# Optimization experiments

Hardware: AMD Instinct MI355X
Metric: run time of the kernel (lower is better)

Reference implementation:

```python
import jax, jax.numpy as jnp
import numpy as np

B, P, C = 1024, 64, 512  # batch, patnum, d_model(channels)
LN_EPS = 1e-5

def setup_inputs() -> dict:
    key = jax.random.key(0)
    k = jax.random.split(key, 5)
    s = 1.0 / np.sqrt(P)  # torch Linear default init scale
    x  = jax.random.normal(k[0], (B, P, C), dtype=jnp.float32)
    W1 = jax.random.uniform(k[1], (C, P, P), minval=-s, maxval=s, dtype=jnp.float32)
    b1 = jax.random.uniform(k[2], (C, P),   minval=-s, maxval=s, dtype=jnp.float32)
    W2 = jax.random.uniform(k[3], (C, P, P), minval=-s, maxval=s, dtype=jnp.float32)
    b2 = jax.random.uniform(k[4], (C, P),   minval=-s, maxval=s, dtype=jnp.float32)
    gamma = jnp.ones((C,), dtype=jnp.float32)   # LayerNorm weight
    beta  = jnp.zeros((C,), dtype=jnp.float32)  # LayerNorm bias
    return {"x": x, "W1": W1, "b1": b1, "W2": W2, "b2": b2, "gamma": gamma, "beta": beta}

def reference(x, W1, b1, W2, b2, gamma, beta):
    # Per-channel Linear over the patch dim, batched across channels.
    # torch Linear: y[q] = sum_p x[p] * W[q, p] + b[q]
    h = jnp.einsum('bpc,cqp->bqc', x, W1) + b1.T[None]          # [B, P, C]
    h = jax.nn.gelu(h, approximate=False)                        # exact GELU (torch default)
    o = jnp.einsum('bpc,cqp->bqc', h, W2) + b2.T[None]          # [B, P, C]
    # Dropout is identity in eval; residual + LayerNorm over channel dim.
    res = o + x
    mean = jnp.mean(res, axis=-1, keepdims=True)
    var = jnp.mean((res - mean) ** 2, axis=-1, keepdims=True)
    return (res - mean) * jax.lax.rsqrt(var + LN_EPS) * gamma + beta
```

## Files before the change

kernel.cpp:

```cpp
#include <hip/hip_runtime.h>
#include <cstdint>
#include <cstddef>

#define BB 1024
#define PP 64
#define CC 512
#define MM (BB * PP)
constexpr float LN_EPS = 1e-5f;

typedef short  s16x8 __attribute__((ext_vector_type(8)));
typedef float  f32x4 __attribute__((ext_vector_type(4)));
typedef unsigned int u32x2 __attribute__((ext_vector_type(2)));

__device__ __forceinline__ unsigned cvt_pk_bf16(float lo, float hi) {
    unsigned r;
    asm("v_cvt_pk_bf16_f32 %0, %1, %2" : "=v"(r) : "v"(lo), "v"(hi));
    return r;
}
__device__ __forceinline__ unsigned cvt_pk_f16(float lo, float hi) {
    unsigned r;
    asm("v_cvt_pkrtz_f16_f32 %0, %1, %2" : "=v"(r) : "v"(lo), "v"(hi));
    return r;
}
__device__ __forceinline__ float h2f(unsigned short h) {
    float f;
    asm("v_cvt_f32_f16 %0, %1" : "=v"(f) : "v"((unsigned)h));
    return f;
}
__device__ __forceinline__ float bflo(unsigned u) { union { unsigned u; float f; } v; v.u = u << 16;          return v.f; }
__device__ __forceinline__ float bfhi(unsigned u) { union { unsigned u; float f; } v; v.u = u & 0xffff0000u;  return v.f; }

__device__ __forceinline__ s16x8 ldwf(const float* p) {
    float4 a = *(const float4*)p;
    float4 b = *(const float4*)(p + 4);
    union { s16x8 v; unsigned u[4]; } r;
    r.u[0] = cvt_pk_bf16(a.x, a.y);
    r.u[1] = cvt_pk_bf16(a.z, a.w);
    r.u[2] = cvt_pk_bf16(b.x, b.y);
    r.u[3] = cvt_pk_bf16(b.z, b.w);
    return r.v;
}

__device__ __forceinline__ float gelu_t(float t) {
    float sg = 1.5957691216f * (t + 0.044715f * t * t * t);
    return t / (1.0f + __expf(-sg));
}

__device__ __forceinline__ void lds_barrier() {
    asm volatile("s_waitcnt lgkmcnt(0)" ::: "memory");
    __builtin_amdgcn_s_barrier();
}

template<int HALF>
__global__ __launch_bounds__(1024, 4) void k_mix_rt(
    const float* __restrict__ X,  const float* __restrict__ W1,
    const float* __restrict__ B1, const float* __restrict__ W2,
    const float* __restrict__ B2, void* __restrict__ RTv)
{
    __shared__ __align__(16) unsigned short XS[16 * 1160];
    __shared__ __align__(16) unsigned short HS[16 * 1152];
    __shared__ __align__(16) float          BS[16 * 128];

    const int tid  = threadIdx.x;
    const int lane = tid & 63;
    const int wv   = tid >> 6;
    const int lb   = lane & 15;
    const int lq   = lane >> 4;

    const int gid = blockIdx.x;
    const int cg  = gid & 31;
    const int bt  = gid >> 5;
    const int c0  = cg * 16, b0 = bt * 128;
    const int c   = c0 + wv;

    const float* w1c = W1 + (size_t)c * 4096;
    const float* w2c = W2 + (size_t)c * 4096;
    const int wq = lb * 64 + lq * 8;
    s16x8 w1_0_0 = ldwf(w1c +    0 + wq), w1_0_1 = ldwf(w1c +    0 + wq + 32);
    s16x8 w1_1_0 = ldwf(w1c + 1024 + wq), w1_1_1 = ldwf(w1c + 1024 + wq + 32);
    s16x8 w1_2_0 = ldwf(w1c + 2048 + wq), w1_2_1 = ldwf(w1c + 2048 + wq + 32);
    s16x8 w1_3_0 = ldwf(w1c + 3072 + wq), w1_3_1 = ldwf(w1c + 3072 + wq + 32);
    s16x8 w2_0_0 = ldwf(w2c +    0 + wq), w2_0_1 = ldwf(w2c +    0 + wq + 32);
    s16x8 w2_1_0 = ldwf(w2c + 1024 + wq), w2_1_1 = ldwf(w2c + 1024 + wq + 32);
    s16x8 w2_2_0 = ldwf(w2c + 2048 + wq), w2_2_1 = ldwf(w2c + 2048 + wq + 32);
    s16x8 w2_3_0 = ldwf(w2c + 3072 + wq), w2_3_1 = ldwf(w2c + 3072 + wq + 32);

    BS[wv * 128 +      lane] = B1[c * 64 + lane];
    BS[wv * 128 + 64 + lane] = B2[c * 64 + lane];

    const unsigned short* xp = &XS[wv * 1160];
    unsigned short*       hp = &HS[wv * 1152];

    const int sc4 = tid & 3;
    const int sp2 = (tid >> 2) & 31;
    const int sbo = tid >> 7;

    float4 r0[2], r1[2];
    #pragma unroll
    for (int pass = 0; pass < 2; ++pass) {
        const float* src = X + ((size_t)(b0 + pass * 8 + sbo) * PP + 2 * sp2) * CC
                             + c0 + sc4 * 4;
        r0[pass] = *(const float4*)src;
        r1[pass] = *(const float4*)(src + CC);
    }

    for (int s = 0; s < 8; ++s) {
        const int bb = b0 + s * 16;

        #pragma unroll
        for (int pass = 0; pass < 2; ++pass) {
            int b = pass * 8 + sbo;
            *(unsigned*)&XS[(sc4 * 4 + 0) * 1160 + b * 72 + 2 * sp2] = cvt_pk_bf16(r0[pass].x, r1[pass].x);
            *(unsigned*)&XS[(sc4 * 4 + 1) * 1160 + b * 72 + 2 * sp2] = cvt_pk_bf16(r0[pass].y, r1[pass].y);
            *(unsigned*)&XS[(sc4 * 4 + 2) * 1160 + b * 72 + 2 * sp2] = cvt_pk_bf16(r0[pass].z, r1[pass].z);
            *(unsigned*)&XS[(sc4 * 4 + 3) * 1160 + b * 72 + 2 * sp2] = cvt_pk_bf16(r0[pass].w, r1[pass].w);
        }

        if (s < 7) {
            #pragma unroll
            for (int pass = 0; pass < 2; ++pass) {
                const float* src = X + ((size_t)(bb + 16 + pass * 8 + sbo) * PP + 2 * sp2) * CC
                                     + c0 + sc4 * 4;
                r0[pass] = *(const float4*)src;
                r1[pass] = *(const float4*)(src + CC);
            }
        }
        lds_barrier();

        s16x8 xf0 = *(const s16x8*)(xp + lb * 72 +  0 + lq * 8);
        s16x8 xf1 = *(const s16x8*)(xp + lb * 72 + 32 + lq * 8);

        #define DO1(mt) { \
            float4 bv = *(const float4*)&BS[wv * 128 + mt * 16 + lq * 4]; \
            f32x4 a = {bv.x, bv.y, bv.z, bv.w}; \
            a = __builtin_amdgcn_mfma_f32_16x16x32_bf16(w1_##mt##_0, xf0, a, 0, 0, 0); \
            a = __builtin_amdgcn_mfma_f32_16x16x32_bf16(w1_##mt##_1, xf1, a, 0, 0, 0); \
            u32x2 hpk; \
            hpk[0] = cvt_pk_bf16(gelu_t(a[0]), gelu_t(a[1])); \
            hpk[1] = cvt_pk_bf16(gelu_t(a[2]), gelu_t(a[3])); \
            *(u32x2*)(hp + lb * 72 + mt * 16 + lq * 4) = hpk; }
        DO1(0) DO1(1) DO1(2) DO1(3)
        #undef DO1

        u32x2 xv0 = *(const u32x2*)(xp + lb * 72 +  0 + lq * 4);
        u32x2 xv1 = *(const u32x2*)(xp + lb * 72 + 16 + lq * 4);
        u32x2 xv2 = *(const u32x2*)(xp + lb * 72 + 32 + lq * 4);
        u32x2 xv3 = *(const u32x2*)(xp + lb * 72 + 48 + lq * 4);

        asm volatile("s_waitcnt lgkmcnt(0)" ::: "memory");

        s16x8 hf0 = *(const s16x8*)(hp + lb * 72 +  0 + lq * 8);
        s16x8 hf1 = *(const s16x8*)(hp + lb * 72 + 32 + lq * 8);

        const size_t rbase = (size_t)c * MM + (size_t)(bb + lb) * 64 + lq * 4;
        #define DO2(mt) { \
            float4 bv = *(const float4*)&BS[wv * 128 + 64 + mt * 16 + lq * 4]; \
            f32x4 a = {bv.x, bv.y, bv.z, bv.w}; \
            a = __builtin_amdgcn_mfma_f32_16x16x32_bf16(w2_##mt##_0, hf0, a, 0, 0, 0); \
            a = __builtin_amdgcn_mfma_f32_16x16x32_bf16(w2_##mt##_1, hf1, a, 0, 0, 0); \
            a[0] += bflo(xv##mt[0]); a[1] += bfhi(xv##mt[0]); \
            a[2] += bflo(xv##mt[1]); a[3] += bfhi(xv##mt[1]); \
            if constexpr (!HALF) { \
                *(f32x4*)((float*)RTv + rbase + mt * 16) = a; \
            } else { \
                u32x2 hv; \
                hv[0] = cvt_pk_f16(a[0], a[1]); \
                hv[1] = cvt_pk_f16(a[2], a[3]); \
                *(u32x2*)((unsigned short*)RTv + rbase + mt * 16) = hv; \
            } }
        DO2(0) DO2(1) DO2(2) DO2(3)
        #undef DO2

        lds_barrier();
    }
}

template<int HALF>
__global__ __launch_bounds__(1024, 4) void k_ln_rt(
    const void* __restrict__ RTv, float* __restrict__ OUT,
    const float* __restrict__ G,  const float* __restrict__ Be)
{
    __shared__ float S[64][516];
    __shared__ float pS[16][64];
    __shared__ float pQ[16][64];
    __shared__ float mu_s[64], inv_s[64];
    __shared__ float gS[512], bS[512];

    const int tid = threadIdx.x;
    const int colbase = blockIdx.x * 64;

    if (tid < 512) gS[tid] = G[tid];
    else           bS[tid - 512] = Be[tid - 512];

    #pragma unroll
    for (int pass = 0; pass < 8; ++pass) {
        const int cc = pass * 64 + (tid >> 4);
        const int ch = (tid & 15) * 4;
        float v0, v1, v2, v3;
        if constexpr (!HALF) {
            f32x4 v = *(const f32x4*)((const float*)RTv + (size_t)cc * MM + colbase + ch);
            v0 = v[0]; v1 = v[1]; v2 = v[2]; v3 = v[3];
        } else {
            u32x2 v = *(const u32x2*)((const unsigned short*)RTv + (size_t)cc * MM + colbase + ch);
            v0 = h2f((unsigned short)(v[0] & 0xffff)); v1 = h2f((unsigned short)(v[0] >> 16));
            v2 = h2f((unsigned short)(v[1] & 0xffff)); v3 = h2f((unsigned short)(v[1] >> 16));
        }
        S[ch + 0][cc] = v0; S[ch + 1][cc] = v1;
        S[ch + 2][cc] = v2; S[ch + 3][cc] = v3;
    }
    __syncthreads();

    const int col = tid >> 4;
    const int cs  = tid & 15;
    float sum = 0.f, sq = 0.f;
    #pragma unroll
    for (int j = 0; j < 32; ++j) {
        float v = S[col][j * 16 + cs];
        sum += v; sq += v * v;
    }
    pS[cs][col] = sum; pQ[cs][col] = sq;
    __syncthreads();

    if (tid < 64) {
        float s = 0.f, q = 0.f;
        #pragma unroll
        for (int k = 0; k < 16; ++k) { s += pS[k][tid]; q += pQ[k][tid]; }
        const float mu  = s * (1.0f / CC);
        const float var = q * (1.0f / CC) - mu * mu;
        mu_s[tid]  = mu;
        inv_s[tid] = rsqrtf(var + LN_EPS);
    }
    __syncthreads();

    const int pos = tid & 7;
    const int hs  = (tid >> 3) & 1;
    const float mu  = mu_s[col];
    const float inv = inv_s[col];
    float* orow = OUT + (size_t)(colbase + col) * CC;
    #pragma unroll
    for (int k = 0; k < 8; ++k) {
        const int cc = hs * 256 + k * 32 + pos * 4;
        f32x4 v = *(const f32x4*)&S[col][cc];
        f32x4 o;
        o[0] = (v[0] - mu) * inv * gS[cc + 0] + bS[cc + 0];
        o[1] = (v[1] - mu) * inv * gS[cc + 1] + bS[cc + 1];
        o[2] = (v[2] - mu) * inv * gS[cc + 2] + bS[cc + 2];
        o[3] = (v[3] - mu) * inv * gS[cc + 3] + bS[cc + 3];
        *(f32x4*)(orow + cc) = o;
    }
}

__global__ __launch_bounds__(1024) void k_mix_legacy(
    const float* __restrict__ X,  const float* __restrict__ W1,
    const float* __restrict__ B1, const float* __restrict__ W2,
    const float* __restrict__ B2, float* __restrict__ OUT)
{
    __shared__ __align__(16) unsigned short XS[16 * 1160];
    __shared__ __align__(16) unsigned short HS[16 * 1152];
    __shared__ __align__(16) float          RS[16 * 1092];
    __shared__ __align__(16) float          BS[16 * 128];

    const int tid  = threadIdx.x;
    const int lane = tid & 63;
    const int wv   = tid >> 6;
    const int lb   = lane & 15;
    const int lq   = lane >> 4;

    const int gid = blockIdx.x;
    const int cg  = gid & 31;
    const int bt  = gid >> 5;
    const int c0  = cg * 16, b0 = bt * 128;
    const int c   = c0 + wv;

    const float* w1c = W1 + (size_t)c * 4096;
    const float* w2c = W2 + (size_t)c * 4096;
    const int wq = lb * 64 + lq * 8;
    s16x8 w1_0_0 = ldwf(w1c +    0 + wq), w1_0_1 = ldwf(w1c +    0 + wq + 32);
    s16x8 w1_1_0 = ldwf(w1c + 1024 + wq), w1_1_1 = ldwf(w1c + 1024 + wq + 32);
    s16x8 w1_2_0 = ldwf(w1c + 2048 + wq), w1_2_1 = ldwf(w1c + 2048 + wq + 32);
    s16x8 w1_3_0 = ldwf(w1c + 3072 + wq), w1_3_1 = ldwf(w1c + 3072 + wq + 32);
    s16x8 w2_0_0 = ldwf(w2c +    0 + wq), w2_0_1 = ldwf(w2c +    0 + wq + 32);
    s16x8 w2_1_0 = ldwf(w2c + 1024 + wq), w2_1_1 = ldwf(w2c + 1024 + wq + 32);
    s16x8 w2_2_0 = ldwf(w2c + 2048 + wq), w2_2_1 = ldwf(w2c + 2048 + wq + 32);
    s16x8 w2_3_0 = ldwf(w2c + 3072 + wq), w2_3_1 = ldwf(w2c + 3072 + wq + 32);

    BS[wv * 128 +      lane] = B1[c * 64 + lane];
    BS[wv * 128 + 64 + lane] = B2[c * 64 + lane];

    const unsigned short* xp = &XS[wv * 1160];
    unsigned short*       hp = &HS[wv * 1152];

    const int sc4 = tid & 3;
    const int sp2 = (tid >> 2) & 31;
    const int sbo = tid >> 7;

    float4 r0[2], r1[2];
    #pragma unroll
    for (int pass = 0; pass < 2; ++pass) {
        const float* src = X + ((size_t)(b0 + pass * 8 + sbo) * PP + 2 * sp2) * CC
                             + c0 + sc4 * 4;
        r0[pass] = *(const float4*)src;
        r1[pass] = *(const float4*)(src + CC);
    }

    for (int s = 0; s < 8; ++s) {
        const int bb = b0 + s * 16;
        #pragma unroll
        for (int pass = 0; pass < 2; ++pass) {
            int b = pass * 8 + sbo;
            *(unsigned*)&XS[(sc4 * 4 + 0) * 1160 + b * 72 + 2 * sp2] = cvt_pk_bf16(r0[pass].x, r1[pass].x);
            *(unsigned*)&XS[(sc4 * 4 + 1) * 1160 + b * 72 + 2 * sp2] = cvt_pk_bf16(r0[pass].y, r1[pass].y);
            *(unsigned*)&XS[(sc4 * 4 + 2) * 1160 + b * 72 + 2 * sp2] = cvt_pk_bf16(r0[pass].z, r1[pass].z);
            *(unsigned*)&XS[(sc4 * 4 + 3) * 1160 + b * 72 + 2 * sp2] = cvt_pk_bf16(r0[pass].w, r1[pass].w);
        }
        __syncthreads();
        if (s < 7) {
            #pragma unroll
            for (int pass = 0; pass < 2; ++pass) {
                const float* src = X + ((size_t)(bb + 16 + pass * 8 + sbo) * PP + 2 * sp2) * CC
                                     + c0 + sc4 * 4;
                r0[pass] = *(const float4*)src;
                r1[pass] = *(const float4*)(src + CC);
            }
        }
        s16x8 xf0 = *(const s16x8*)(xp + lb * 72 +  0 + lq * 8);
        s16x8 xf1 = *(const s16x8*)(xp + lb * 72 + 32 + lq * 8);
        #define DO1(mt) { \
            float4 bv = *(const float4*)&BS[wv * 128 + mt * 16 + lq * 4]; \
            f32x4 a = {bv.x, bv.y, bv.z, bv.w}; \
            a = __builtin_amdgcn_mfma_f32_16x16x32_bf16(w1_##mt##_0, xf0, a, 0, 0, 0); \
            a = __builtin_amdgcn_mfma_f32_16x16x32_bf16(w1_##mt##_1, xf1, a, 0, 0, 0); \
            u32x2 hpk; \
            hpk[0] = cvt_pk_bf16(gelu_t(a[0]), gelu_t(a[1])); \
            hpk[1] = cvt_pk_bf16(gelu_t(a[2]), gelu_t(a[3])); \
            *(u32x2*)(hp + lb * 72 + mt * 16 + lq * 4) = hpk; }
        DO1(0) DO1(1) DO1(2) DO1(3)
        #undef DO1
        asm volatile("s_waitcnt lgkmcnt(0)" ::: "memory");
        s16x8 hf0 = *(const s16x8*)(hp + lb * 72 +  0 + lq * 8);
        s16x8 hf1 = *(const s16x8*)(hp + lb * 72 + 32 + lq * 8);
        #define DO2(mt) { \
            float4 bv = *(const float4*)&BS[wv * 128 + 64 + mt * 16 + lq * 4]; \
            f32x4 a = {bv.x, bv.y, bv.z, bv.w}; \
            a = __builtin_amdgcn_mfma_f32_16x16x32_bf16(w2_##mt##_0, hf0, a, 0, 0, 0); \
            a = __builtin_amdgcn_mfma_f32_16x16x32_bf16(w2_##mt##_1, hf1, a, 0, 0, 0); \
            u32x2 xv = *(const u32x2*)(xp + lb * 72 + mt * 16 + lq * 4); \
            a[0] += bflo(xv[0]); a[1] += bfhi(xv[0]); \
            a[2] += bflo(xv[1]); a[3] += bfhi(xv[1]); \
            *(f32x4*)&RS[lb * 1092 + wv * 68 + mt * 16 + lq * 4] = a; }
        DO2(0) DO2(1) DO2(2) DO2(3)
        #undef DO2
        __syncthreads();
        #pragma unroll
        for (int it = 0; it < 4; ++it) {
            int fi = it * 1024 + tid;
            int c4 = fi & 3, q = (fi >> 2) & 63, b = fi >> 8;
            const float* rp = &RS[b * 1092 + c4 * 4 * 68 + q];
            float4 v = { rp[0], rp[68], rp[136], rp[204] };
            *(float4*)(OUT + ((size_t)(bb + b) * PP + q) * CC + c0 + c4 * 4) = v;
        }
    }
}

__global__ __launch_bounds__(256) void k_ln_legacy(
    float* __restrict__ OUT, const float* __restrict__ G, const float* __restrict__ Be)
{
    const int lane = threadIdx.x & 63;
    const int m    = blockIdx.x * 4 + (threadIdx.x >> 6);
    float4* row = (float4*)(OUT + (size_t)m * CC);
    float4 v0 = row[lane], v1 = row[lane + 64];
    float s = (v0.x + v0.y) + (v0.z + v0.w) + (v1.x + v1.y) + (v1.z + v1.w);
    float q = (v0.x * v0.x + v0.y * v0.y) + (v0.z * v0.z + v0.w * v0.w)
            + (v1.x * v1.x + v1.y * v1.y) + (v1.z * v1.z + v1.w * v1.w);
    #pragma unroll
    for (int o = 32; o >= 1; o >>= 1) {
        s += __shfl_xor(s, o, 64);
        q += __shfl_xor(q, o, 64);
    }
    const float mu  = s * (1.0f / CC);
    const float var = q * (1.0f / CC) - mu * mu;
    const float inv = rsqrtf(var + LN_EPS);
    const float4 g0 = ((const float4*)G)[lane],  g1 = ((const float4*)G)[lane + 64];
    const float4 e0 = ((const float4*)Be)[lane], e1 = ((const float4*)Be)[lane + 64];
    v0.x = (v0.x - mu) * inv * g0.x + e0.x;  v0.y = (v0.y - mu) * inv * g0.y + e0.y;
    v0.z = (v0.z - mu) * inv * g0.z + e0.z;  v0.w = (v0.w - mu) * inv * g0.w + e0.w;
    v1.x = (v1.x - mu) * inv * g1.x + e1.x;  v1.y = (v1.y - mu) * inv * g1.y + e1.y;
    v1.z = (v1.z - mu) * inv * g1.z + e1.z;  v1.w = (v1.w - mu) * inv * g1.w + e1.w;
    row[lane] = v0; row[lane + 64] = v1;
}

extern "C" void kernel_launch(void* const* d_in, const int* in_sizes, int n_in,
                              void* d_out, int out_size, void* d_ws, size_t ws_size,
                              hipStream_t stream) {
    const float* X  = (const float*)d_in[0];
    const float* W1 = (const float*)d_in[1];
    const float* B1 = (const float*)d_in[2];
    const float* W2 = (const float*)d_in[3];
    const float* B2 = (const float*)d_in[4];
    const float* G  = (const float*)d_in[5];
    const float* Be = (const float*)d_in[6];
    float* OUT = (float*)d_out;

    const size_t need32 = (size_t)CC * MM * sizeof(float);
    const size_t need16 = (size_t)CC * MM * sizeof(unsigned short);

    if (d_ws && ws_size >= need32) {
        k_mix_rt<0><<<256, 1024, 0, stream>>>(X, W1, B1, W2, B2, d_ws);
        k_ln_rt<0><<<MM / 64, 1024, 0, stream>>>(d_ws, OUT, G, Be);
    } else if (d_ws && ws_size >= need16) {
        k_mix_rt<1><<<256, 1024, 0, stream>>>(X, W1, B1, W2, B2, d_ws);
        k_ln_rt<1><<<MM / 64, 1024, 0, stream>>>(d_ws, OUT, G, Be);
    } else {
        k_mix_legacy<<<256, 1024, 0, stream>>>(X, W1, B1, W2, B2, OUT);
        k_ln_legacy<<<MM / 4, 256, 0, stream>>>(OUT, G, Be);
    }
}
```

Measured before the change: 339.9 us.

## Pre-transpose X to channel-major bf16 in a separate kernel before the mixer

Adds a transpose kernel that converts X to bf16 and writes it channel-major into the workspace. The mixer then reads each channel's activations straight from global memory instead of staging them through shared memory, which removes the LDS staging and the block barriers. The mixer block shrinks to 4 waves with biases kept in registers. The cost is an extra kernel launch plus an extra write and read of a 64 MB bf16 intermediate. The transpose's strided 2-byte global stores may also be poorly coalesced.

```diff
diff --git a/kernel.cpp b/kernel.cpp
--- a/kernel.cpp
+++ b/kernel.cpp
@@ -46,20 +46,40 @@
     return t / (1.0f + __expf(-sg));
 }
 
-__device__ __forceinline__ void lds_barrier() {
-    asm volatile("s_waitcnt lgkmcnt(0)" ::: "memory");
-    __builtin_amdgcn_s_barrier();
+__global__ __launch_bounds__(1024, 4) void k_tr(
+    const float* __restrict__ X, unsigned short* __restrict__ XT)
+{
+    __shared__ unsigned short S[64 * 514];
+    const int tid = threadIdx.x;
+    const int mb  = blockIdx.x;
+    const int rg  = tid >> 7;
+    const int c0  = (tid & 127) * 4;
+
+    #pragma unroll
+    for (int it = 0; it < 8; ++it) {
+        const int m = it * 8 + rg;
+        float4 v = *(const float4*)(X + (size_t)(mb * 64 + m) * CC + c0);
+        unsigned* p = (unsigned*)&S[m * 514 + c0];
+        p[0] = cvt_pk_bf16(v.x, v.y);
+        p[1] = cvt_pk_bf16(v.z, v.w);
+    }
+    __syncthreads();
+
+    const int wv = tid >> 6, lane = tid & 63;
+    unsigned short* dst = XT + (size_t)(wv * 32) * MM + mb * 64 + lane;
+    #pragma unroll
+    for (int j = 0; j < 32; ++j) {
+        dst[(size_t)j * MM] = S[lane * 514 + wv * 32 + j];
+    }
 }
 
 template<int HALF>
-__global__ __launch_bounds__(1024, 4) void k_mix_rt(
-    const float* __restrict__ X,  const float* __restrict__ W1,
+__global__ __launch_bounds__(256, 3) void k_mix_rt(
+    const unsigned short* __restrict__ XT, const float* __restrict__ W1,
     const float* __restrict__ B1, const float* __restrict__ W2,
     const float* __restrict__ B2, void* __restrict__ RTv)
 {
-    __shared__ __align__(16) unsigned short XS[16 * 1160];
-    __shared__ __align__(16) unsigned short HS[16 * 1152];
-    __shared__ __align__(16) float          BS[16 * 128];
+    __shared__ __align__(16) unsigned short HS[4][1152];
 
     const int tid  = threadIdx.x;
     const int lane = tid & 63;
@@ -68,10 +88,10 @@
     const int lq   = lane >> 4;
 
     const int gid = blockIdx.x;
-    const int cg  = gid & 31;
-    const int bt  = gid >> 5;
-    const int c0  = cg * 16, b0 = bt * 128;
-    const int c   = c0 + wv;
+    const int cgi = gid & 127;
+    const int bt  = gid >> 7;
+    const int c   = cgi * 4 + wv;
+    const int b0  = bt * 128;
 
     const float* w1c = W1 + (size_t)c * 4096;
     const float* w2c = W2 + (size_t)c * 4096;
@@ -84,55 +104,31 @@
     s16x8 w2_1_0 = ldwf(w2c + 1024 + wq), w2_1_1 = ldwf(w2c + 1024 + wq + 32);
     s16x8 w2_2_0 = ldwf(w2c + 2048 + wq), w2_2_1 = ldwf(w2c + 2048 + wq + 32);
     s16x8 w2_3_0 = ldwf(w2c + 3072 + wq), w2_3_1 = ldwf(w2c + 3072 + wq + 32);
-
-    BS[wv * 128 +      lane] = B1[c * 64 + lane];
-    BS[wv * 128 + 64 + lane] = B2[c * 64 + lane];
-
-    const unsigned short* xp = &XS[wv * 1160];
-    unsigned short*       hp = &HS[wv * 1152];
-
-    const int sc4 = tid & 3;
-    const int sp2 = (tid >> 2) & 31;
-    const int sbo = tid >> 7;
-
-    float4 r0[2], r1[2];
-    #pragma unroll
-    for (int pass = 0; pass < 2; ++pass) {
-        const float* src = X + ((size_t)(b0 + pass * 8 + sbo) * PP + 2 * sp2) * CC
-                             + c0 + sc4 * 4;
-        r0[pass] = *(const float4*)src;
-        r1[pass] = *(const float4*)(src + CC);
-    }
+    const float4 b1_0 = *(const float4*)(B1 + c * 64 +  0 + lq * 4);
+    const float4 b1_1 = *(const float4*)(B1 + c * 64 + 16 + lq * 4);
+    const float4 b1_2 = *(const float4*)(B1 + c * 64 + 32 + lq * 4);
+    const float4 b1_3 = *(const float4*)(B1 + c * 64 + 48 + lq * 4);
+    const float4 b2_0 = *(const float4*)(B2 + c * 64 +  0 + lq * 4);
+    const float4 b2_1 = *(const float4*)(B2 + c * 64 + 16 + lq * 4);
+    const float4 b2_2 = *(const float4*)(B2 + c * 64 + 32 + lq * 4);
+    const float4 b2_3 = *(const float4*)(B2 + c * 64 + 48 + lq * 4);
+
+    const unsigned short* xtc = XT + (size_t)c * MM;
+    unsigned short*       hp  = &HS[wv][0];
 
     for (int s = 0; s < 8; ++s) {
         const int bb = b0 + s * 16;
-
-        #pragma unroll
-        for (int pass = 0; pass < 2; ++pass) {
-            int b = pass * 8 + sbo;
-            *(unsigned*)&XS[(sc4 * 4 + 0) * 1160 + b * 72 + 2 * sp2] = cvt_pk_bf16(r0[pass].x, r1[pass].x);
-            *(unsigned*)&XS[(sc4 * 4 + 1) * 1160 + b * 72 + 2 * sp2] = cvt_pk_bf16(r0[pass].y, r1[pass].y);
-            *(unsigned*)&XS[(sc4 * 4 + 2) * 1160 + b * 72 + 2 * sp2] = cvt_pk_bf16(r0[pass].z, r1[pass].z);
-            *(unsigned*)&XS[(sc4 * 4 + 3) * 1160 + b * 72 + 2 * sp2] = cvt_pk_bf16(r0[pass].w, r1[pass].w);
-        }
-
-        if (s < 7) {
-            #pragma unroll
-            for (int pass = 0; pass < 2; ++pass) {
-                const float* src = X + ((size_t)(bb + 16 + pass * 8 + sbo) * PP + 2 * sp2) * CC
-                                     + c0 + sc4 * 4;
-                r0[pass] = *(const float4*)src;
-                r1[pass] = *(const float4*)(src + CC);
-            }
-        }
-        lds_barrier();
-
-        s16x8 xf0 = *(const s16x8*)(xp + lb * 72 +  0 + lq * 8);
-        s16x8 xf1 = *(const s16x8*)(xp + lb * 72 + 32 + lq * 8);
+        const unsigned short* xrow = xtc + (size_t)(bb + lb) * 64;
+
+        s16x8 xf0 = *(const s16x8*)(xrow +      lq * 8);
+        s16x8 xf1 = *(const s16x8*)(xrow + 32 + lq * 8);
+        u32x2 xv0 = *(const u32x2*)(xrow +  0 + lq * 4);
+        u32x2 xv1 = *(const u32x2*)(xrow + 16 + lq * 4);
+        u32x2 xv2 = *(const u32x2*)(xrow + 32 + lq * 4);
+        u32x2 xv3 = *(const u32x2*)(xrow + 48 + lq * 4);
 
         #define DO1(mt) { \
-            float4 bv = *(const float4*)&BS[wv * 128 + mt * 16 + lq * 4]; \
-            f32x4 a = {bv.x, bv.y, bv.z, bv.w}; \
+            f32x4 a = {b1_##mt.x, b1_##mt.y, b1_##mt.z, b1_##mt.w}; \
             a = __builtin_amdgcn_mfma_f32_16x16x32_bf16(w1_##mt##_0, xf0, a, 0, 0, 0); \
             a = __builtin_amdgcn_mfma_f32_16x16x32_bf16(w1_##mt##_1, xf1, a, 0, 0, 0); \
             u32x2 hpk; \
@@ -142,11 +138,6 @@
         DO1(0) DO1(1) DO1(2) DO1(3)
         #undef DO1
 
-        u32x2 xv0 = *(const u32x2*)(xp + lb * 72 +  0 + lq * 4);
-        u32x2 xv1 = *(const u32x2*)(xp + lb * 72 + 16 + lq * 4);
-        u32x2 xv2 = *(const u32x2*)(xp + lb * 72 + 32 + lq * 4);
-        u32x2 xv3 = *(const u32x2*)(xp + lb * 72 + 48 + lq * 4);
-
         asm volatile("s_waitcnt lgkmcnt(0)" ::: "memory");
 
         s16x8 hf0 = *(const s16x8*)(hp + lb * 72 +  0 + lq * 8);
@@ -154,8 +145,7 @@
 
         const size_t rbase = (size_t)c * MM + (size_t)(bb + lb) * 64 + lq * 4;
         #define DO2(mt) { \
-            float4 bv = *(const float4*)&BS[wv * 128 + 64 + mt * 16 + lq * 4]; \
-            f32x4 a = {bv.x, bv.y, bv.z, bv.w}; \
+            f32x4 a = {b2_##mt.x, b2_##mt.y, b2_##mt.z, b2_##mt.w}; \
             a = __builtin_amdgcn_mfma_f32_16x16x32_bf16(w2_##mt##_0, hf0, a, 0, 0, 0); \
             a = __builtin_amdgcn_mfma_f32_16x16x32_bf16(w2_##mt##_1, hf1, a, 0, 0, 0); \
             a[0] += bflo(xv##mt[0]); a[1] += bfhi(xv##mt[0]); \
@@ -170,8 +160,6 @@
             } }
         DO2(0) DO2(1) DO2(2) DO2(3)
         #undef DO2
-
-        lds_barrier();
     }
 }
 
@@ -401,15 +389,22 @@
     const float* Be = (const float*)d_in[6];
     float* OUT = (float*)d_out;
 
-    const size_t need32 = (size_t)CC * MM * sizeof(float);
-    const size_t need16 = (size_t)CC * MM * sizeof(unsigned short);
-
-    if (d_ws && ws_size >= need32) {
-        k_mix_rt<0><<<256, 1024, 0, stream>>>(X, W1, B1, W2, B2, d_ws);
-        k_ln_rt<0><<<MM / 64, 1024, 0, stream>>>(d_ws, OUT, G, Be);
-    } else if (d_ws && ws_size >= need16) {
-        k_mix_rt<1><<<256, 1024, 0, stream>>>(X, W1, B1, W2, B2, d_ws);
-        k_ln_rt<1><<<MM / 64, 1024, 0, stream>>>(d_ws, OUT, G, Be);
+    const size_t xt_bytes = (size_t)CC * MM * sizeof(unsigned short);
+    const size_t rt32     = (size_t)CC * MM * sizeof(float);
+    const size_t rt16     = xt_bytes;
+
+    if (d_ws && ws_size >= xt_bytes + rt32) {
+        unsigned short* XT = (unsigned short*)d_ws;
+        float* RT = (float*)((char*)d_ws + xt_bytes);
+        k_tr<<<MM / 64, 1024, 0, stream>>>(X, XT);
+        k_mix_rt<0><<<1024, 256, 0, stream>>>(XT, W1, B1, W2, B2, RT);
+        k_ln_rt<0><<<MM / 64, 1024, 0, stream>>>(RT, OUT, G, Be);
+    } else if (d_ws && ws_size >= xt_bytes + rt16) {
+        unsigned short* XT = (unsigned short*)d_ws;
+        unsigned short* RT = (unsigned short*)((char*)d_ws + xt_bytes);
+        k_tr<<<MM / 64, 1024, 0, stream>>>(X, XT);
+        k_mix_rt<1><<<1024, 256, 0, stream>>>(XT, W1, B1, W2, B2, RT);
+        k_ln_rt<1><<<MM / 64, 1024, 0, stream>>>(RT, OUT, G, Be);
     } else {
         k_mix_legacy<<<256, 1024, 0, stream>>>(X, W1, B1, W2, B2, OUT);
         k_ln_legacy<<<MM / 4, 256, 0, stream>>>(OUT, G, Be);
```

Measured after the change: 366.7 us. 1.08x slower.

## Use fp16 intermediate buffer always, halve mix block work, shrink LDS

Applied to the files above, without the earlier changes.

The intermediate residual tensor is now always written as fp16 instead of fp32 when workspace allows, which halves the write and read traffic between the mix and LayerNorm kernels. The mix kernel launches 512 blocks of 64 batches each instead of 256 blocks of 128, so more blocks are available to fill the CUs. Biases are kept in LDS as bf16. The LN kernel stores fp16 in LDS to cut LDS usage and raise occupancy. This costs precision in the intermediate and in the biases, and the weight loads are amortized over fewer batch steps per block.

```diff
diff --git a/kernel.cpp b/kernel.cpp
--- a/kernel.cpp
+++ b/kernel.cpp
@@ -51,15 +51,14 @@
     __builtin_amdgcn_s_barrier();
 }
 
-template<int HALF>
-__global__ __launch_bounds__(1024, 4) void k_mix_rt(
+__global__ __launch_bounds__(1024, 8) void k_mix_rt16(
     const float* __restrict__ X,  const float* __restrict__ W1,
     const float* __restrict__ B1, const float* __restrict__ W2,
-    const float* __restrict__ B2, void* __restrict__ RTv)
+    const float* __restrict__ B2, unsigned short* __restrict__ RT)
 {
     __shared__ __align__(16) unsigned short XS[16 * 1160];
     __shared__ __align__(16) unsigned short HS[16 * 1152];
-    __shared__ __align__(16) float          BS[16 * 128];
+    __shared__ unsigned BSu[16][64];
 
     const int tid  = threadIdx.x;
     const int lane = tid & 63;
@@ -70,7 +69,7 @@
     const int gid = blockIdx.x;
     const int cg  = gid & 31;
     const int bt  = gid >> 5;
-    const int c0  = cg * 16, b0 = bt * 128;
+    const int c0  = cg * 16, b0 = bt * 64;
     const int c   = c0 + wv;
 
     const float* w1c = W1 + (size_t)c * 4096;
@@ -85,8 +84,12 @@
     s16x8 w2_2_0 = ldwf(w2c + 2048 + wq), w2_2_1 = ldwf(w2c + 2048 + wq + 32);
     s16x8 w2_3_0 = ldwf(w2c + 3072 + wq), w2_3_1 = ldwf(w2c + 3072 + wq + 32);
 
-    BS[wv * 128 +      lane] = B1[c * 64 + lane];
-    BS[wv * 128 + 64 + lane] = B2[c * 64 + lane];
+    {
+        const int ch = tid >> 6, j = tid & 63;
+        const float* bsrc = (j < 32) ? (B1 + (c0 + ch) * 64 + 2 * j)
+                                     : (B2 + (c0 + ch) * 64 + 2 * (j - 32));
+        BSu[ch][j] = cvt_pk_bf16(bsrc[0], bsrc[1]);
+    }
 
     const unsigned short* xp = &XS[wv * 1160];
     unsigned short*       hp = &HS[wv * 1152];
@@ -104,7 +107,7 @@
         r1[pass] = *(const float4*)(src + CC);
     }
 
-    for (int s = 0; s < 8; ++s) {
+    for (int s = 0; s < 4; ++s) {
         const int bb = b0 + s * 16;
 
         #pragma unroll
@@ -116,7 +119,7 @@
             *(unsigned*)&XS[(sc4 * 4 + 3) * 1160 + b * 72 + 2 * sp2] = cvt_pk_bf16(r0[pass].w, r1[pass].w);
         }
 
-        if (s < 7) {
+        if (s < 3) {
             #pragma unroll
             for (int pass = 0; pass < 2; ++pass) {
                 const float* src = X + ((size_t)(bb + 16 + pass * 8 + sbo) * PP + 2 * sp2) * CC
@@ -131,8 +134,8 @@
         s16x8 xf1 = *(const s16x8*)(xp + lb * 72 + 32 + lq * 8);
 
         #define DO1(mt) { \
-            float4 bv = *(const float4*)&BS[wv * 128 + mt * 16 + lq * 4]; \
-            f32x4 a = {bv.x, bv.y, bv.z, bv.w}; \
+            u32x2 bp = *(const u32x2*)&BSu[wv][mt * 8 + lq * 2]; \
+            f32x4 a = {bflo(bp[0]), bfhi(bp[0]), bflo(bp[1]), bfhi(bp[1])}; \
             a = __builtin_amdgcn_mfma_f32_16x16x32_bf16(w1_##mt##_0, xf0, a, 0, 0, 0); \
             a = __builtin_amdgcn_mfma_f32_16x16x32_bf16(w1_##mt##_1, xf1, a, 0, 0, 0); \
             u32x2 hpk; \
@@ -154,20 +157,16 @@
 
         const size_t rbase = (size_t)c * MM + (size_t)(bb + lb) * 64 + lq * 4;
         #define DO2(mt) { \
-            float4 bv = *(const float4*)&BS[wv * 128 + 64 + mt * 16 + lq * 4]; \
-            f32x4 a = {bv.x, bv.y, bv.z, bv.w}; \
+            u32x2 bp = *(const u32x2*)&BSu[wv][32 + mt * 8 + lq * 2]; \
+            f32x4 a = {bflo(bp[0]), bfhi(bp[0]), bflo(bp[1]), bfhi(bp[1])}; \
             a = __builtin_amdgcn_mfma_f32_16x16x32_bf16(w2_##mt##_0, hf0, a, 0, 0, 0); \
             a = __builtin_amdgcn_mfma_f32_16x16x32_bf16(w2_##mt##_1, hf1, a, 0, 0, 0); \
             a[0] += bflo(xv##mt[0]); a[1] += bfhi(xv##mt[0]); \
             a[2] += bflo(xv##mt[1]); a[3] += bfhi(xv##mt[1]); \
-            if constexpr (!HALF) { \
-                *(f32x4*)((float*)RTv + rbase + mt * 16) = a; \
-            } else { \
-                u32x2 hv; \
-                hv[0] = cvt_pk_f16(a[0], a[1]); \
-                hv[1] = cvt_pk_f16(a[2], a[3]); \
-                *(u32x2*)((unsigned short*)RTv + rbase + mt * 16) = hv; \
-            } }
+            u32x2 hv; \
+            hv[0] = cvt_pk_f16(a[0], a[1]); \
+            hv[1] = cvt_pk_f16(a[2], a[3]); \
+            *(u32x2*)(RT + rbase + mt * 16) = hv; }
         DO2(0) DO2(1) DO2(2) DO2(3)
         #undef DO2
 
@@ -175,12 +174,11 @@
     }
 }
 
-template<int HALF>
-__global__ __launch_bounds__(1024, 4) void k_ln_rt(
-    const void* __restrict__ RTv, float* __restrict__ OUT,
+__global__ __launch_bounds__(1024, 8) void k_ln_rt16(
+    const unsigned short* __restrict__ RT, float* __restrict__ OUT,
     const float* __restrict__ G,  const float* __restrict__ Be)
 {
-    __shared__ float S[64][516];
+    __shared__ unsigned short S[64][520];
     __shared__ float pS[16][64];
     __shared__ float pQ[16][64];
     __shared__ float mu_s[64], inv_s[64];
@@ -196,17 +194,11 @@
     for (int pass = 0; pass < 8; ++pass) {
         const int cc = pass * 64 + (tid >> 4);
         const int ch = (tid & 15) * 4;
-        float v0, v1, v2, v3;
-        if constexpr (!HALF) {
-            f32x4 v = *(const f32x4*)((const float*)RTv + (size_t)cc * MM + colbase + ch);
-            v0 = v[0]; v1 = v[1]; v2 = v[2]; v3 = v[3];
-        } else {
-            u32x2 v = *(const u32x2*)((const unsigned short*)RTv + (size_t)cc * MM + colbase + ch);
-            v0 = h2f((unsigned short)(v[0] & 0xffff)); v1 = h2f((unsigned short)(v[0] >> 16));
-            v2 = h2f((unsigned short)(v[1] & 0xffff)); v3 = h2f((unsigned short)(v[1] >> 16));
-        }
-        S[ch + 0][cc] = v0; S[ch + 1][cc] = v1;
-        S[ch + 2][cc] = v2; S[ch + 3][cc] = v3;
+        u32x2 v = *(const u32x2*)(RT + (size_t)cc * MM + colbase + ch);
+        S[ch + 0][cc] = (unsigned short)(v[0] & 0xffffu);
+        S[ch + 1][cc] = (unsigned short)(v[0] >> 16);
+        S[ch + 2][cc] = (unsigned short)(v[1] & 0xffffu);
+        S[ch + 3][cc] = (unsigned short)(v[1] >> 16);
     }
     __syncthreads();
 
@@ -215,7 +207,7 @@
     float sum = 0.f, sq = 0.f;
     #pragma unroll
     for (int j = 0; j < 32; ++j) {
-        float v = S[col][j * 16 + cs];
+        float v = h2f(S[col][j * 16 + cs]);
         sum += v; sq += v * v;
     }
     pS[cs][col] = sum; pQ[cs][col] = sq;
@@ -232,21 +224,20 @@
     }
     __syncthreads();
 
-    const int pos = tid & 7;
-    const int hs  = (tid >> 3) & 1;
+    const int pos = tid & 15;
     const float mu  = mu_s[col];
     const float inv = inv_s[col];
     float* orow = OUT + (size_t)(colbase + col) * CC;
     #pragma unroll
     for (int k = 0; k < 8; ++k) {
-        const int cc = hs * 256 + k * 32 + pos * 4;
-        f32x4 v = *(const f32x4*)&S[col][cc];
-        f32x4 o;
-        o[0] = (v[0] - mu) * inv * gS[cc + 0] + bS[cc + 0];
-        o[1] = (v[1] - mu) * inv * gS[cc + 1] + bS[cc + 1];
-        o[2] = (v[2] - mu) * inv * gS[cc + 2] + bS[cc + 2];
-        o[3] = (v[3] - mu) * inv * gS[cc + 3] + bS[cc + 3];
-        *(f32x4*)(orow + cc) = o;
+        const int cc = k * 64 + pos * 4;
+        u32x2 v = *(const u32x2*)&S[col][cc];
+        float4 o;
+        o.x = (h2f((unsigned short)(v[0] & 0xffffu)) - mu) * inv * gS[cc + 0] + bS[cc + 0];
+        o.y = (h2f((unsigned short)(v[0] >> 16))     - mu) * inv * gS[cc + 1] + bS[cc + 1];
+        o.z = (h2f((unsigned short)(v[1] & 0xffffu)) - mu) * inv * gS[cc + 2] + bS[cc + 2];
+        o.w = (h2f((unsigned short)(v[1] >> 16))     - mu) * inv * gS[cc + 3] + bS[cc + 3];
+        *(float4*)(orow + cc) = o;
     }
 }
 
@@ -401,15 +392,12 @@
     const float* Be = (const float*)d_in[6];
     float* OUT = (float*)d_out;
 
-    const size_t need32 = (size_t)CC * MM * sizeof(float);
-    const size_t need16 = (size_t)CC * MM * sizeof(unsigned short);
-
-    if (d_ws && ws_size >= need32) {
-        k_mix_rt<0><<<256, 1024, 0, stream>>>(X, W1, B1, W2, B2, d_ws);
-        k_ln_rt<0><<<MM / 64, 1024, 0, stream>>>(d_ws, OUT, G, Be);
-    } else if (d_ws && ws_size >= need16) {
-        k_mix_rt<1><<<256, 1024, 0, stream>>>(X, W1, B1, W2, B2, d_ws);
-        k_ln_rt<1><<<MM / 64, 1024, 0, stream>>>(d_ws, OUT, G, Be);
+    const size_t rt16 = (size_t)CC * MM * sizeof(unsigned short);
+
+    if (d_ws && ws_size >= rt16) {
+        unsigned short* RT = (unsigned short*)d_ws;
+        k_mix_rt16<<<512, 1024, 0, stream>>>(X, W1, B1, W2, B2, RT);
+        k_ln_rt16<<<MM / 64, 1024, 0, stream>>>(RT, OUT, G, Be);
     } else {
         k_mix_legacy<<<256, 1024, 0, stream>>>(X, W1, B1, W2, B2, OUT);
         k_ln_legacy<<<MM / 4, 256, 0, stream>>>(OUT, G, Be);
```

New measurement: 430.5 us. 1.27x slower.
